# Kernel tuning notes

Measured on AMD Instinct MI355X. Metric: run time of the kernel, lower is better.

## Reference

```python
import jax, jax.numpy as jnp
import numpy as np

N_COLORS = 3  # color1..color3 occupy z[:, 3:6]


def setup_inputs() -> dict:
    key = jax.random.key(0)
    k1, k2 = jax.random.split(key)
    B, D = 4194304, 8
    z = jax.random.normal(k1, (B, D), dtype=jnp.float32)
    a = jax.random.uniform(k2, (B, N_COLORS), dtype=jnp.float32)
    return {"z": z, "a": a}


def reference(z, a):
    # Vectorized equivalent of the per-row loop: argmax over the color slice,
    # one-hot it, mask with a, and reduce over the color axis.
    colors = z[:, 3:6]                                   # [B, 3]
    z_color = jax.nn.one_hot(jnp.argmax(colors, axis=1), N_COLORS, dtype=z.dtype)
    return (a * z_color).sum(axis=1)                     # [B]
```

## Files before the change

### kernel.cpp

```cpp
#include <hip/hip_runtime.h>
#include <hip/hip_bf16.h>


#define ROWS_PER_BLOCK 512
#define NTHREADS 256

typedef float nfloat4 __attribute__((ext_vector_type(4)));
typedef float nfloat2 __attribute__((ext_vector_type(2)));

__global__ __launch_bounds__(NTHREADS) void color_val_lds(
    const float* __restrict__ z,
    const float* __restrict__ a,
    float* __restrict__ out)
{
    __shared__ float zc[ROWS_PER_BLOCK * 3];
    __shared__ __align__(16) float as_[ROWS_PER_BLOCK * 3];

    const int t = threadIdx.x;
    const size_t rowBase = (size_t)blockIdx.x * ROWS_PER_BLOCK;

    const nfloat4* zg = reinterpret_cast<const nfloat4*>(z) + rowBase * 2;
#pragma unroll
    for (int q = 0; q < 4; ++q) {
        int f = q * NTHREADS + t;
        nfloat4 v = __builtin_nontemporal_load(&zg[f]);
        int r = f >> 1;
        int odd = f & 1;
        zc[r * 3 + odd] = odd ? v[0] : v[3];
        if (odd) zc[r * 3 + 2] = v[1];
    }

    const nfloat2* ag = reinterpret_cast<const nfloat2*>(a) + (rowBase * 3) / 2;
    nfloat2* as2 = reinterpret_cast<nfloat2*>(as_);
#pragma unroll
    for (int q = 0; q < 3; ++q) {
        int p2 = q * NTHREADS + t;
        as2[p2] = __builtin_nontemporal_load(&ag[p2]);
    }

    __syncthreads();

#pragma unroll
    for (int k = 0; k < 2; ++k) {
        int r = k * NTHREADS + t;
        float c0 = zc[r * 3 + 0];
        float c1 = zc[r * 3 + 1];
        float c2 = zc[r * 3 + 2];
        const float* ar = &as_[r * 3];
        float val = ar[0];
        float m = c0;
        if (c1 > m) { m = c1; val = ar[1]; }
        if (c2 > m) {          val = ar[2]; }
        __builtin_nontemporal_store(val, &out[rowBase + r]);
    }
}

__global__ void color_val_tail(
    const float* __restrict__ z,
    const float* __restrict__ a,
    float* __restrict__ out,
    size_t start, size_t B)
{
    size_t i = start + blockIdx.x * blockDim.x + threadIdx.x;
    if (i >= B) return;
    float c0 = z[i * 8 + 3], c1 = z[i * 8 + 4], c2 = z[i * 8 + 5];
    float val = a[i * 3 + 0];
    float m = c0;
    if (c1 > m) { m = c1; val = a[i * 3 + 1]; }
    if (c2 > m) {          val = a[i * 3 + 2]; }
    out[i] = val;
}

extern "C" void kernel_launch(void* const* d_in, const int* in_sizes, int n_in,
                              void* d_out, int out_size, void* d_ws, size_t ws_size,
                              hipStream_t stream) {
    const float* z = (const float*)d_in[0];
    const float* a = (const float*)d_in[1];
    float* out = (float*)d_out;

    size_t B = (size_t)out_size;
    size_t nfull = B / ROWS_PER_BLOCK;
    size_t rem = B % ROWS_PER_BLOCK;

    if (nfull > 0)
        color_val_lds<<<(int)nfull, NTHREADS, 0, stream>>>(z, a, out);
    if (rem > 0) {
        size_t start = nfull * ROWS_PER_BLOCK;
        int blocks = (int)((rem + 255) / 256);
        color_val_tail<<<blocks, 256, 0, stream>>>(z, a, out, start, B);
    }
}
```

Measured before the change: 34.41 us.

## Replace LDS staging and block barrier with wave shuffles and gathered a loads

Each wave handles 64 rows independently. Pairs of lanes exchange the color components of each row via xor shuffles, compute the argmax, then load only the selected element of a with a per-lane gather. Results are compacted with shuffles into one coalesced store. This removes shared memory and __syncthreads, but it replaces the vectorized coalesced loads of a with scattered scalar loads that still touch the same cache lines.

```diff
diff --git a/kernel.cpp b/kernel.cpp
--- a/kernel.cpp
+++ b/kernel.cpp
@@ -2,57 +2,47 @@
 #include <hip/hip_bf16.h>
 
 
-#define ROWS_PER_BLOCK 512
 #define NTHREADS 256
 
 typedef float nfloat4 __attribute__((ext_vector_type(4)));
-typedef float nfloat2 __attribute__((ext_vector_type(2)));
 
-__global__ __launch_bounds__(NTHREADS) void color_val_lds(
+__global__ __launch_bounds__(NTHREADS) void color_val_shfl(
     const float* __restrict__ z,
     const float* __restrict__ a,
-    float* __restrict__ out)
+    float* __restrict__ out,
+    size_t nwaves)
 {
-    __shared__ float zc[ROWS_PER_BLOCK * 3];
-    __shared__ __align__(16) float as_[ROWS_PER_BLOCK * 3];
+    const int lane = threadIdx.x & 63;
+    const size_t wave = ((size_t)blockIdx.x * (NTHREADS / 64)) + (threadIdx.x >> 6);
+    if (wave >= nwaves) return;
 
-    const int t = threadIdx.x;
-    const size_t rowBase = (size_t)blockIdx.x * ROWS_PER_BLOCK;
+    const size_t R0 = wave * 64;
+    const nfloat4* zg = reinterpret_cast<const nfloat4*>(z) + R0 * 2;
 
-    const nfloat4* zg = reinterpret_cast<const nfloat4*>(z) + rowBase * 2;
+    float res[2];
 #pragma unroll
-    for (int q = 0; q < 4; ++q) {
-        int f = q * NTHREADS + t;
-        nfloat4 v = __builtin_nontemporal_load(&zg[f]);
-        int r = f >> 1;
-        int odd = f & 1;
-        zc[r * 3 + odd] = odd ? v[0] : v[3];
-        if (odd) zc[r * 3 + 2] = v[1];
+    for (int rd = 0; rd < 2; ++rd) {
+        nfloat4 v = __builtin_nontemporal_load(&zg[rd * 64 + lane]);
+        float o0 = __shfl_xor(v[0], 1);
+        float o1 = __shfl_xor(v[1], 1);
+        float o3 = __shfl_xor(v[3], 1);
+        bool odd = lane & 1;
+        float c0 = odd ? o3 : v[3];
+        float c1 = odd ? v[0] : o0;
+        float c2 = odd ? v[1] : o1;
+        int j = 0;
+        float m = c0;
+        if (c1 > m) { m = c1; j = 1; }
+        if (c2 > m) {          j = 2; }
+        size_t row = R0 + (size_t)rd * 32 + (lane >> 1);
+        res[rd] = a[row * 3 + j];
     }
 
-    const nfloat2* ag = reinterpret_cast<const nfloat2*>(a) + (rowBase * 3) / 2;
-    nfloat2* as2 = reinterpret_cast<nfloat2*>(as_);
-#pragma unroll
-    for (int q = 0; q < 3; ++q) {
-        int p2 = q * NTHREADS + t;
-        as2[p2] = __builtin_nontemporal_load(&ag[p2]);
-    }
-
-    __syncthreads();
-
-#pragma unroll
-    for (int k = 0; k < 2; ++k) {
-        int r = k * NTHREADS + t;
-        float c0 = zc[r * 3 + 0];
-        float c1 = zc[r * 3 + 1];
-        float c2 = zc[r * 3 + 2];
-        const float* ar = &as_[r * 3];
-        float val = ar[0];
-        float m = c0;
-        if (c1 > m) { m = c1; val = ar[1]; }
-        if (c2 > m) {          val = ar[2]; }
-        __builtin_nontemporal_store(val, &out[rowBase + r]);
-    }
+    int src = (2 * lane) & 63;
+    float rA = __shfl(res[0], src);
+    float rB = __shfl(res[1], src);
+    float r = (lane < 32) ? rA : rB;
+    __builtin_nontemporal_store(r, &out[R0 + lane]);
 }
 
 __global__ void color_val_tail(
@@ -79,13 +69,16 @@
     float* out = (float*)d_out;
 
     size_t B = (size_t)out_size;
-    size_t nfull = B / ROWS_PER_BLOCK;
-    size_t rem = B % ROWS_PER_BLOCK;
+    size_t nwaves = B / 64;
+    size_t rem = B % 64;
 
-    if (nfull > 0)
-        color_val_lds<<<(int)nfull, NTHREADS, 0, stream>>>(z, a, out);
+    if (nwaves > 0) {
+        int wavesPerBlock = NTHREADS / 64;
+        int blocks = (int)((nwaves + wavesPerBlock - 1) / wavesPerBlock);
+        color_val_shfl<<<blocks, NTHREADS, 0, stream>>>(z, a, out, nwaves);
+    }
     if (rem > 0) {
-        size_t start = nfull * ROWS_PER_BLOCK;
+        size_t start = nwaves * 64;
         int blocks = (int)((rem + 255) / 256);
         color_val_tail<<<blocks, 256, 0, stream>>>(z, a, out, start, B);
     }
```

Measured after the change: 35.20 us. +2.3%, slower.

## Convert to persistent grid with register double-buffered tile prefetch

Applied to the files above, without the earlier changes.

Replaces the one-block-per-tile launch with a fixed grid of 2048 persistent blocks that stride over tiles. Each block prefetches the next tile's z and a data into registers while staging the current tile through shared memory and computing it. The aim is to hide global-load latency and cut block launch overhead on a memory-bound streaming kernel. In exchange it doubles register use for the staging buffers and adds extra barriers per tile, which may lower occupancy.

```diff
diff --git a/kernel.cpp b/kernel.cpp
--- a/kernel.cpp
+++ b/kernel.cpp
@@ -4,54 +4,93 @@
 
 #define ROWS_PER_BLOCK 512
 #define NTHREADS 256
+#define NBLOCKS 2048
 
 typedef float nfloat4 __attribute__((ext_vector_type(4)));
 typedef float nfloat2 __attribute__((ext_vector_type(2)));
 
-__global__ __launch_bounds__(NTHREADS) void color_val_lds(
+__global__ __launch_bounds__(NTHREADS) void color_val_pipe(
     const float* __restrict__ z,
     const float* __restrict__ a,
-    float* __restrict__ out)
+    float* __restrict__ out,
+    int ntiles)
 {
     __shared__ float zc[ROWS_PER_BLOCK * 3];
     __shared__ __align__(16) float as_[ROWS_PER_BLOCK * 3];
+    nfloat2* as2 = reinterpret_cast<nfloat2*>(as_);
 
     const int t = threadIdx.x;
-    const size_t rowBase = (size_t)blockIdx.x * ROWS_PER_BLOCK;
+    const int G = gridDim.x;
 
-    const nfloat4* zg = reinterpret_cast<const nfloat4*>(z) + rowBase * 2;
+    nfloat4 vzA[4], vzB[4];
+    nfloat2 vaA[3], vaB[3];
+
+    auto loadT = [&](nfloat4 (&vz)[4], nfloat2 (&va)[3], int tile) {
+        const nfloat4* zg = reinterpret_cast<const nfloat4*>(z)
+                            + (size_t)tile * ROWS_PER_BLOCK * 2;
 #pragma unroll
-    for (int q = 0; q < 4; ++q) {
-        int f = q * NTHREADS + t;
-        nfloat4 v = __builtin_nontemporal_load(&zg[f]);
-        int r = f >> 1;
-        int odd = f & 1;
-        zc[r * 3 + odd] = odd ? v[0] : v[3];
-        if (odd) zc[r * 3 + 2] = v[1];
-    }
+        for (int q = 0; q < 4; ++q)
+            vz[q] = __builtin_nontemporal_load(&zg[q * NTHREADS + t]);
+        const nfloat2* ag = reinterpret_cast<const nfloat2*>(a)
+                            + (size_t)tile * (ROWS_PER_BLOCK * 3 / 2);
+#pragma unroll
+        for (int q = 0; q < 3; ++q)
+            va[q] = __builtin_nontemporal_load(&ag[q * NTHREADS + t]);
+    };
 
-    const nfloat2* ag = reinterpret_cast<const nfloat2*>(a) + (rowBase * 3) / 2;
-    nfloat2* as2 = reinterpret_cast<nfloat2*>(as_);
+    auto writeLds = [&](nfloat4 (&vz)[4], nfloat2 (&va)[3]) {
 #pragma unroll
-    for (int q = 0; q < 3; ++q) {
-        int p2 = q * NTHREADS + t;
-        as2[p2] = __builtin_nontemporal_load(&ag[p2]);
-    }
+        for (int q = 0; q < 4; ++q) {
+            int f = q * NTHREADS + t;
+            int r = f >> 1;
+            int odd = f & 1;
+            zc[r * 3 + odd] = odd ? vz[q][0] : vz[q][3];
+            if (odd) zc[r * 3 + 2] = vz[q][1];
+        }
+#pragma unroll
+        for (int q = 0; q < 3; ++q)
+            as2[q * NTHREADS + t] = va[q];
+    };
 
-    __syncthreads();
+    auto computeT = [&](int tile) {
+        size_t rowBase = (size_t)tile * ROWS_PER_BLOCK;
+#pragma unroll
+        for (int k = 0; k < 2; ++k) {
+            int r = k * NTHREADS + t;
+            float c0 = zc[r * 3 + 0];
+            float c1 = zc[r * 3 + 1];
+            float c2 = zc[r * 3 + 2];
+            const float* ar = &as_[r * 3];
+            float val = ar[0];
+            float m = c0;
+            if (c1 > m) { m = c1; val = ar[1]; }
+            if (c2 > m) {          val = ar[2]; }
+            __builtin_nontemporal_store(val, &out[rowBase + r]);
+        }
+    };
 
-#pragma unroll
-    for (int k = 0; k < 2; ++k) {
-        int r = k * NTHREADS + t;
-        float c0 = zc[r * 3 + 0];
-        float c1 = zc[r * 3 + 1];
-        float c2 = zc[r * 3 + 2];
-        const float* ar = &as_[r * 3];
-        float val = ar[0];
-        float m = c0;
-        if (c1 > m) { m = c1; val = ar[1]; }
-        if (c2 > m) {          val = ar[2]; }
-        __builtin_nontemporal_store(val, &out[rowBase + r]);
+    int tile = blockIdx.x;
+    if (tile >= ntiles) return;
+    loadT(vzA, vaA, tile);
+
+    for (;;) {
+        int tB = tile + G;
+        if (tB < ntiles) loadT(vzB, vaB, tB);
+        __syncthreads();
+        writeLds(vzA, vaA);
+        __syncthreads();
+        computeT(tile);
+        if (tB >= ntiles) break;
+        tile = tB;
+
+        int tA = tile + G;
+        if (tA < ntiles) loadT(vzA, vaA, tA);
+        __syncthreads();
+        writeLds(vzB, vaB);
+        __syncthreads();
+        computeT(tile);
+        if (tA >= ntiles) break;
+        tile = tA;
     }
 }
 
@@ -79,13 +118,15 @@
     float* out = (float*)d_out;
 
     size_t B = (size_t)out_size;
-    size_t nfull = B / ROWS_PER_BLOCK;
+    size_t ntiles = B / ROWS_PER_BLOCK;
     size_t rem = B % ROWS_PER_BLOCK;
 
-    if (nfull > 0)
-        color_val_lds<<<(int)nfull, NTHREADS, 0, stream>>>(z, a, out);
+    if (ntiles > 0) {
+        int grid = (int)(ntiles < NBLOCKS ? ntiles : NBLOCKS);
+        color_val_pipe<<<grid, NTHREADS, 0, stream>>>(z, a, out, (int)ntiles);
+    }
     if (rem > 0) {
-        size_t start = nfull * ROWS_PER_BLOCK;
+        size_t start = ntiles * ROWS_PER_BLOCK;
         int blocks = (int)((rem + 255) / 256);
         color_val_tail<<<blocks, 256, 0, stream>>>(z, a, out, start, B);
     }
```

Result: slower. 37.32 us (+8.5%).
